# Performance work log

Hardware: AMD Instinct MI355X
Metric: run time of the kernel (lower is better)

Reference implementation:

```python
import jax, jax.numpy as jnp
from jax import lax
import numpy as np

B, T, F, H, MH = 512, 256, 8, 128, 512  # batch, horizon, exo features, lstm hidden, mlp hidden


def setup_inputs() -> dict:
    key = jax.random.key(0)
    ks = jax.random.split(key, 32)

    def u(k, shape, scale):
        return jax.random.uniform(k, shape, jnp.float32, -scale, scale)

    kH = 1.0 / np.sqrt(H)
    kM = 1.0 / np.sqrt(MH)
    inp = {}
    for i, n in enumerate(["Dis_out", "Dis_rad", "Dis_occ"]):
        inp[n] = jax.random.normal(ks[i], (B, T, F), jnp.float32)
    for j in range(3):
        b = 3 + j * 5
        inp[f"lstm{j+1}_Wih"] = u(ks[b], (4 * H, F), kH)      # torch gate order i,f,g,o
        inp[f"lstm{j+1}_Whh"] = u(ks[b + 1], (4 * H, H), kH)
        inp[f"lstm{j+1}_b"] = u(ks[b + 2], (4 * H,), kH)
        inp[f"lstm{j+1}_hw"] = u(ks[b + 3], (H,), kH)          # linear head H -> 1
        inp[f"lstm{j+1}_hb"] = u(ks[b + 4], (), kH)
    inp["mlp_W1"] = u(ks[20], (3, MH), 1.0 / np.sqrt(3.0))
    inp["mlp_b1"] = u(ks[21], (MH,), 1.0 / np.sqrt(3.0))
    inp["mlp_W2"] = u(ks[22], (MH, MH), kM)
    inp["mlp_b2"] = u(ks[23], (MH,), kM)
    inp["mlp_W3"] = u(ks[24], (MH,), kM)
    inp["mlp_b3"] = u(ks[25], (), kM)
    return inp


def _lstm_head(x, Wih, Whh, b, hw, hb):
    # x: (B,T,F) -> per-step scalar prediction (B,T)
    Bsz, Hs = x.shape[0], Whh.shape[1]

    def step(carry, xt):
        h, c = carry
        z = xt @ Wih.T + h @ Whh.T + b                 # (B,4H)
        i, f, g, o = jnp.split(z, 4, axis=-1)
        c = jax.nn.sigmoid(f) * c + jax.nn.sigmoid(i) * jnp.tanh(g)
        h = jax.nn.sigmoid(o) * jnp.tanh(c)
        return (h, c), h

    h0 = jnp.zeros((Bsz, Hs), x.dtype)
    _, hs = lax.scan(step, (h0, h0), jnp.swapaxes(x, 0, 1))  # hs: (T,B,H)
    return jnp.einsum('tbh,h->bt', hs, hw) + hb              # (B,T)


def reference(Dis_out, Dis_rad, Dis_occ,
              lstm1_Wih, lstm1_Whh, lstm1_b, lstm1_hw, lstm1_hb,
              lstm2_Wih, lstm2_Whh, lstm2_b, lstm2_hw, lstm2_hb,
              lstm3_Wih, lstm3_Whh, lstm3_b, lstm3_hw, lstm3_hb,
              mlp_W1, mlp_b1, mlp_W2, mlp_b2, mlp_W3, mlp_b3):
    D1 = _lstm_head(Dis_out, lstm1_Wih, lstm1_Whh, lstm1_b, lstm1_hw, lstm1_hb)
    D2 = _lstm_head(Dis_rad, lstm2_Wih, lstm2_Whh, lstm2_b, lstm2_hw, lstm2_hb)
    D3 = _lstm_head(Dis_occ, lstm3_Wih, lstm3_Whh, lstm3_b, lstm3_hw, lstm3_hb)
    # Batched replacement of the per-timestep loop: concat -> tiny MLP, all T at once.
    x = jnp.stack([D1, D2, D3], axis=-1)                      # (B,T,3)
    h = jax.nn.relu(x @ mlp_W1 + mlp_b1)                      # (B,T,MH)
    h = jax.nn.relu(h @ mlp_W2 + mlp_b2)                      # (B,T,MH)
    c_p_F = h @ mlp_W3 + mlp_b3                               # (B,T)
    return (D1, D2, D3, c_p_F)
```

## Files before the change

kernel.cpp:

```cpp
#include <hip/hip_runtime.h>

#define B_ 512
#define T_ 256
#define F_ 8
#define H_ 128
#define BT_ (B_*T_)
#define MH_ 512
#define L2E 1.4426950408889634f

typedef __attribute__((ext_vector_type(4))) float f32x4;
typedef __attribute__((ext_vector_type(8))) __bf16 bf16x8;

__device__ unsigned short g_w2t[MH_*MH_];
__device__ unsigned short g_whh[3][512][128];
__device__ unsigned short g_wih[3][512][32];
__device__ unsigned short g_xbf[3][B_*T_*F_];

__device__ __forceinline__ unsigned short f2bf(float f){
  unsigned int u = __float_as_uint(f);
  unsigned int r = (u + 0x7FFFu + ((u >> 16) & 1u)) >> 16;
  return (unsigned short)r;
}

#if __has_builtin(__builtin_amdgcn_exp2f)
#define EXP2F __builtin_amdgcn_exp2f
#else
#define EXP2F exp2f
#endif
#define RCPF __builtin_amdgcn_rcpf

struct LstmArgs {
  const float* x[3];
  const float* Wih[3];
  const float* Whh[3];
  const float* bias[3];
  const float* hw[3];
  const float* hb[3];
  float* out;
};

__global__ __launch_bounds__(256) void prep_lstm(LstmArgs A){
  const int NW = 3*512*128;
  const int NI = 3*512*32;
  const int NX = 3*B_*T_*F_;
  for (int i = blockIdx.x*256 + threadIdx.x; i < NW+NI+NX; i += gridDim.x*256){
    if (i < NW){
      int head = i >> 16;
      int r = i & 65535;
      int pc = r >> 7, k = r & 127;
      int w = pc >> 6, g = (pc >> 4) & 3, s = pc & 15;
      int row = g*128 + w*16 + s;
      float sc = (g == 2) ? (2.0f*L2E) : (-L2E);
      g_whh[head][pc][k] = f2bf(A.Whh[head][row*H_ + k] * sc);
    } else if (i < NW + NI){
      int j = i - NW;
      int head = j >> 14;
      int r = j & 16383;
      int pc = r >> 5, k = r & 31;
      int w = pc >> 6, g = (pc >> 4) & 3, s = pc & 15;
      int row = g*128 + w*16 + s;
      float sc = (g == 2) ? (2.0f*L2E) : (-L2E);
      g_wih[head][pc][k] = (k < 8) ? f2bf(A.Wih[head][row*F_ + k] * sc) : (unsigned short)0;
    } else {
      int j = i - NW - NI;
      int head = j >> 20;
      int r = j & 1048575;
      g_xbf[head][r] = f2bf(A.x[head][r]);
    }
  }
}

__global__ __launch_bounds__(512) void lstm_mfma_kernel(LstmArgs A){
  const int head   = blockIdx.x >> 6;
  const int batch0 = (blockIdx.x & 63) * 8;
  const int tid = threadIdx.x;
  const int w   = tid >> 6;
  const int l   = tid & 63;
  const int c16 = l & 15;
  const int kb  = (l >> 4) * 8;

  const float* __restrict__ bs  = A.bias[head];
  const float* __restrict__ hwp = A.hw[head];
  const float hbv = A.hb[head][0];
  float* __restrict__ D = A.out + (size_t)head * BT_;

  bf16x8 bh[4][4];
  bf16x8 bx[4];
  #pragma unroll
  for (int g = 0; g < 4; ++g){
    const int pc = w*64 + g*16 + c16;
    #pragma unroll
    for (int kk = 0; kk < 4; ++kk)
      bh[g][kk] = *(const bf16x8*)&g_whh[head][pc][kk*32 + kb];
    bx[g] = *(const bf16x8*)&g_wih[head][pc][kb];
  }

  const int u = w*16 + c16;
  const float bi_ = bs[u]        * (-L2E);
  const float bf_ = bs[H_+u]     * (-L2E);
  const float bg_ = bs[2*H_+u]   * (2.0f*L2E);
  const float bo_ = bs[3*H_+u]   * (-L2E);
  const float hw_u = hwp[u];

  __shared__ __align__(16) unsigned short h_bf[2][16][132];
  __shared__ float part[2][8][8];

  for (int i = tid; i < 2*16*132; i += 512) ((unsigned short*)h_bf)[i] = 0;

  float cst[2] = {0.f, 0.f};
  float pp[2]  = {0.f, 0.f};

  const int bt = ((c16 >> 2) << 1) | (c16 & 1);
  const bool xvalid = (l < 16) && !(l & 2);
  const unsigned short* __restrict__ xrow =
      &g_xbf[head][(size_t)(batch0 + bt) * (T_*F_)];

  bf16x8 ax_cur = {};
  if (xvalid) ax_cur = *(const bf16x8*)(xrow);

  __syncthreads();

  int cur = 0;
  for (int ts = 0; ts < T_; ++ts){
    bf16x8 ah[4];
    #pragma unroll
    for (int kk = 0; kk < 4; ++kk)
      ah[kk] = *(const bf16x8*)&h_bf[cur][c16][kk*32 + kb];

    bf16x8 ax_nxt = {};
    {
      const int tn = (ts + 1 < T_) ? ts + 1 : ts;
      if (xvalid) ax_nxt = *(const bf16x8*)(xrow + tn*F_);
    }

    f32x4 acc[4];
    const f32x4 z4 = {0.f, 0.f, 0.f, 0.f};
    #pragma unroll
    for (int g = 0; g < 4; ++g)
      acc[g] = __builtin_amdgcn_mfma_f32_16x16x32_bf16(ah[0], bh[g][0], z4, 0, 0, 0);
    #pragma unroll
    for (int kk = 1; kk < 4; ++kk){
      #pragma unroll
      for (int g = 0; g < 4; ++g)
        acc[g] = __builtin_amdgcn_mfma_f32_16x16x32_bf16(ah[kk], bh[g][kk], acc[g], 0, 0, 0);
    }
    #pragma unroll
    for (int g = 0; g < 4; ++g)
      acc[g] = __builtin_amdgcn_mfma_f32_16x16x32_bf16(ax_cur, bx[g], acc[g], 0, 0, 0);

    if (ts > 0){
      #pragma unroll
      for (int r = 0; r < 2; ++r){
        float v = pp[r];
        v += __shfl_xor(v, 1); v += __shfl_xor(v, 2);
        v += __shfl_xor(v, 4); v += __shfl_xor(v, 8);
        if (c16 == 0) part[(ts-1) & 1][(l >> 4)*2 + r][w] = v;
      }
    }

    #pragma unroll
    for (int r = 0; r < 2; ++r){
      const float Zi = acc[0][r] + bi_;
      const float Zf = acc[1][r] + bf_;
      const float Zg = acc[2][r] + bg_;
      const float Zo = acc[3][r] + bo_;
      const float si = RCPF(1.f + EXP2F(Zi));
      const float sf = RCPF(1.f + EXP2F(Zf));
      const float tg = 1.f - 2.f * RCPF(EXP2F(Zg) + 1.f);
      const float so = RCPF(1.f + EXP2F(Zo));
      cst[r] = sf * cst[r] + si * tg;
      const float tc = 1.f - 2.f * RCPF(EXP2F(cst[r] * (2.0f*L2E)) + 1.f);
      const float hnr = so * tc;
      h_bf[cur ^ 1][(l >> 4)*4 + r][u] = f2bf(hnr);
      pp[r] = hnr * hw_u;
    }

    __syncthreads();

    if (ts > 0 && tid < 64){
      const int b  = tid >> 3;
      const int wv = tid & 7;
      float v = part[(ts-1) & 1][b][wv];
      v += __shfl_xor(v, 1); v += __shfl_xor(v, 2); v += __shfl_xor(v, 4);
      if (wv == 0) D[(size_t)(batch0 + b) * T_ + (ts-1)] = v + hbv;
    }

    ax_cur = ax_nxt;
    cur ^= 1;
  }

  #pragma unroll
  for (int r = 0; r < 2; ++r){
    float v = pp[r];
    v += __shfl_xor(v, 1); v += __shfl_xor(v, 2);
    v += __shfl_xor(v, 4); v += __shfl_xor(v, 8);
    if (c16 == 0) part[(T_-1) & 1][(l >> 4)*2 + r][w] = v;
  }
  __syncthreads();
  if (tid < 64){
    const int b  = tid >> 3;
    const int wv = tid & 7;
    float v = part[(T_-1) & 1][b][wv];
    v += __shfl_xor(v, 1); v += __shfl_xor(v, 2); v += __shfl_xor(v, 4);
    if (wv == 0) D[(size_t)(batch0 + b) * T_ + (T_-1)] = v + hbv;
  }
}

__global__ __launch_bounds__(256) void prep_w2t(const float* __restrict__ W2){
  const int idx = blockIdx.x * 256 + threadIdx.x;
  const int n = idx >> 9;
  const int k = idx & 511;
  g_w2t[(n << 9) | (k ^ ((n & 7) << 3))] = f2bf(W2[(size_t)k * MH_ + n]);
}

__global__ __launch_bounds__(256, 2) void mlp_kernel(
    const float* __restrict__ Dbase,
    const float* __restrict__ W1, const float* __restrict__ b1,
    const float* __restrict__ b2, const float* __restrict__ W3,
    const float* __restrict__ b3, float* __restrict__ out)
{
  __shared__ __align__(16) unsigned short buf[2][32*512];

  const int tid = threadIdx.x;
  const int l   = tid & 63;
  const int c16 = l & 15;
  const int kb  = (l >> 4) * 8;
  const int w   = tid >> 6;
  const int m0  = blockIdx.x * 128 + w * 32;

  bf16x8 afr[2][16];
  {
    float d[2][3];
    #pragma unroll
    for (int mt = 0; mt < 2; ++mt){
      const int gr = m0 + mt*16 + c16;
      d[mt][0] = Dbase[gr];
      d[mt][1] = Dbase[BT_ + gr];
      d[mt][2] = Dbase[2*BT_ + gr];
    }
    #pragma unroll
    for (int ks = 0; ks < 16; ++ks){
      const int kg = ks*32 + kb;
      const f32x4 wa0 = *(const f32x4*)(W1 + kg);          const f32x4 wa1 = *(const f32x4*)(W1 + kg + 4);
      const f32x4 wb0 = *(const f32x4*)(W1 + MH_ + kg);    const f32x4 wb1 = *(const f32x4*)(W1 + MH_ + kg + 4);
      const f32x4 wc0 = *(const f32x4*)(W1 + 2*MH_ + kg);  const f32x4 wc1 = *(const f32x4*)(W1 + 2*MH_ + kg + 4);
      const f32x4 bv0 = *(const f32x4*)(b1 + kg);          const f32x4 bv1 = *(const f32x4*)(b1 + kg + 4);
      #pragma unroll
      for (int mt = 0; mt < 2; ++mt){
        union { unsigned short us[8]; bf16x8 v; } au;
        #pragma unroll
        for (int i = 0; i < 4; ++i){
          float v0 = fmaf(d[mt][2], wc0[i], fmaf(d[mt][1], wb0[i], fmaf(d[mt][0], wa0[i], bv0[i])));
          float v1 = fmaf(d[mt][2], wc1[i], fmaf(d[mt][1], wb1[i], fmaf(d[mt][0], wa1[i], bv1[i])));
          au.us[i]     = f2bf(fmaxf(v0, 0.f));
          au.us[4 + i] = f2bf(fmaxf(v1, 0.f));
        }
        afr[mt][ks] = au.v;
      }
    }
  }

  const uint4* __restrict__ gsrc = (const uint4*)g_w2t;
  uint4 rg0, rg1, rg2, rg3, rg4, rg5, rg6, rg7;
  {
    const uint4* s = gsrc + tid;
    rg0 = s[0*256]; rg1 = s[1*256]; rg2 = s[2*256]; rg3 = s[3*256];
    rg4 = s[4*256]; rg5 = s[5*256]; rg6 = s[6*256]; rg7 = s[7*256];
  }

  float rs[2][4] = {{0.f,0.f,0.f,0.f},{0.f,0.f,0.f,0.f}};

  #pragma unroll 1
  for (int p = 0; p < 16; ++p){
    {
      uint4* bw = (uint4*)buf[p & 1] + tid;
      bw[0*256] = rg0; bw[1*256] = rg1; bw[2*256] = rg2; bw[3*256] = rg3;
      bw[4*256] = rg4; bw[5*256] = rg5; bw[6*256] = rg6; bw[7*256] = rg7;
    }
    __syncthreads();
    if (p < 15){
      const uint4* s = gsrc + (p + 1) * 2048 + tid;
      rg0 = s[0*256]; rg1 = s[1*256]; rg2 = s[2*256]; rg3 = s[3*256];
      rg4 = s[4*256]; rg5 = s[5*256]; rg6 = s[6*256]; rg7 = s[7*256];
    }
    float b2v[2], w3v[2];
    #pragma unroll
    for (int nt = 0; nt < 2; ++nt){
      const int n = p*32 + nt*16 + c16;
      b2v[nt] = b2[n];
      w3v[nt] = W3[n];
    }

    const unsigned short* __restrict__ bb = buf[p & 1];
    f32x4 acc[2][2];
    #pragma unroll
    for (int nt = 0; nt < 2; ++nt){
      f32x4 z = {0.f,0.f,0.f,0.f};
      acc[0][nt] = z; acc[1][nt] = z;
    }
    #pragma unroll
    for (int ks = 0; ks < 16; ++ks){
      #pragma unroll
      for (int nt = 0; nt < 2; ++nt){
        const int nl = nt*16 + c16;
        const bf16x8 bfr =
          *(const bf16x8*)&bb[(nl << 9) | ((ks*32 + kb) ^ ((nl & 7) << 3))];
        acc[0][nt] = __builtin_amdgcn_mfma_f32_16x16x32_bf16(afr[0][ks], bfr, acc[0][nt], 0, 0, 0);
        acc[1][nt] = __builtin_amdgcn_mfma_f32_16x16x32_bf16(afr[1][ks], bfr, acc[1][nt], 0, 0, 0);
      }
    }
    #pragma unroll
    for (int nt = 0; nt < 2; ++nt){
      #pragma unroll
      for (int mt = 0; mt < 2; ++mt)
        #pragma unroll
        for (int r = 0; r < 4; ++r)
          rs[mt][r] += fmaxf(acc[mt][nt][r] + b2v[nt], 0.f) * w3v[nt];
    }
  }

  #pragma unroll
  for (int mt = 0; mt < 2; ++mt){
    #pragma unroll
    for (int r = 0; r < 4; ++r){
      rs[mt][r] += __shfl_xor(rs[mt][r], 1);
      rs[mt][r] += __shfl_xor(rs[mt][r], 2);
      rs[mt][r] += __shfl_xor(rs[mt][r], 4);
      rs[mt][r] += __shfl_xor(rs[mt][r], 8);
    }
  }
  if (c16 == 0){
    const float bv = b3[0];
    #pragma unroll
    for (int mt = 0; mt < 2; ++mt){
      const int row = m0 + mt*16 + (l >> 4) * 4;
      #pragma unroll
      for (int r = 0; r < 4; ++r)
        out[3*BT_ + row + r] = rs[mt][r] + bv;
    }
  }
}

extern "C" void kernel_launch(void* const* d_in, const int* in_sizes, int n_in,
                              void* d_out, int out_size, void* d_ws, size_t ws_size,
                              hipStream_t stream){
  LstmArgs A;
  for (int i = 0; i < 3; ++i){
    A.x[i]    = (const float*)d_in[i];
    A.Wih[i]  = (const float*)d_in[3 + i*5 + 0];
    A.Whh[i]  = (const float*)d_in[3 + i*5 + 1];
    A.bias[i] = (const float*)d_in[3 + i*5 + 2];
    A.hw[i]   = (const float*)d_in[3 + i*5 + 3];
    A.hb[i]   = (const float*)d_in[3 + i*5 + 4];
  }
  A.out = (float*)d_out;

  prep_w2t<<<dim3(1024), dim3(256), 0, stream>>>((const float*)d_in[20]);
  prep_lstm<<<dim3(2048), dim3(256), 0, stream>>>(A);
  lstm_mfma_kernel<<<dim3(192), dim3(512), 0, stream>>>(A);
  mlp_kernel<<<dim3(1024), dim3(256), 0, stream>>>((const float*)d_out,
      (const float*)d_in[18], (const float*)d_in[19],
      (const float*)d_in[21], (const float*)d_in[22], (const float*)d_in[23],
      (float*)d_out);
}
```

Baseline: 329.5 us.

## Compute LSTM head projection via MFMA in wave 0 and fold bias into accumulators

Replaces the per-step shuffle reduction plus shared-memory partial-sum stage for the linear head with an extra MFMA chain in wave 0. That chain multiplies the bf16 hidden state just read from LDS by a padded bf16 head-weight matrix, and the head bias is used as the initial accumulator. Gate biases are likewise preloaded into the MFMA accumulators, and the bf16 conversion uses the hardware cast. This removes the shuffles, the partial-sum buffer and the post-barrier reduction from the serial recurrence. The cost is some imbalance, since wave 0 does extra MFMA work, and the head now sees h in bf16 instead of fp32.

```diff
diff --git a/kernel.cpp b/kernel.cpp
--- a/kernel.cpp
+++ b/kernel.cpp
@@ -15,11 +15,17 @@
 __device__ unsigned short g_whh[3][512][128];
 __device__ unsigned short g_wih[3][512][32];
 __device__ unsigned short g_xbf[3][B_*T_*F_];
+__device__ unsigned short g_hwd[3][16][128];
 
 __device__ __forceinline__ unsigned short f2bf(float f){
   unsigned int u = __float_as_uint(f);
   unsigned int r = (u + 0x7FFFu + ((u >> 16) & 1u)) >> 16;
   return (unsigned short)r;
+}
+__device__ __forceinline__ unsigned short cvt_bf16(float f){
+  union { __bf16 b; unsigned short u; } c;
+  c.b = (__bf16)f;
+  return c.u;
 }
 
 #if __has_builtin(__builtin_amdgcn_exp2f)
@@ -43,7 +49,8 @@
   const int NW = 3*512*128;
   const int NI = 3*512*32;
   const int NX = 3*B_*T_*F_;
-  for (int i = blockIdx.x*256 + threadIdx.x; i < NW+NI+NX; i += gridDim.x*256){
+  const int NH = 3*16*128;
+  for (int i = blockIdx.x*256 + threadIdx.x; i < NW+NI+NX+NH; i += gridDim.x*256){
     if (i < NW){
       int head = i >> 16;
       int r = i & 65535;
@@ -61,11 +68,17 @@
       int row = g*128 + w*16 + s;
       float sc = (g == 2) ? (2.0f*L2E) : (-L2E);
       g_wih[head][pc][k] = (k < 8) ? f2bf(A.Wih[head][row*F_ + k] * sc) : (unsigned short)0;
-    } else {
+    } else if (i < NW + NI + NX){
       int j = i - NW - NI;
       int head = j >> 20;
       int r = j & 1048575;
       g_xbf[head][r] = f2bf(A.x[head][r]);
+    } else {
+      int j = i - NW - NI - NX;
+      int head = j >> 11;
+      int r = j & 2047;
+      int col = r >> 7, k = r & 127;
+      g_hwd[head][col][k] = (col == 0) ? f2bf(A.hw[head][k]) : (unsigned short)0;
     }
   }
 }
@@ -80,7 +93,6 @@
   const int kb  = (l >> 4) * 8;
 
   const float* __restrict__ bs  = A.bias[head];
-  const float* __restrict__ hwp = A.hw[head];
   const float hbv = A.hb[head][0];
   float* __restrict__ D = A.out + (size_t)head * BT_;
 
@@ -94,38 +106,47 @@
       bh[g][kk] = *(const bf16x8*)&g_whh[head][pc][kk*32 + kb];
     bx[g] = *(const bf16x8*)&g_wih[head][pc][kb];
   }
+  bf16x8 bD[4];
+  if (w == 0){
+    #pragma unroll
+    for (int kk = 0; kk < 4; ++kk)
+      bD[kk] = *(const bf16x8*)&g_hwd[head][c16][kk*32 + kb];
+  }
 
   const int u = w*16 + c16;
   const float bi_ = bs[u]        * (-L2E);
   const float bf_ = bs[H_+u]     * (-L2E);
   const float bg_ = bs[2*H_+u]   * (2.0f*L2E);
   const float bo_ = bs[3*H_+u]   * (-L2E);
-  const float hw_u = hwp[u];
 
   __shared__ __align__(16) unsigned short h_bf[2][16][132];
-  __shared__ float part[2][8][8];
 
   for (int i = tid; i < 2*16*132; i += 512) ((unsigned short*)h_bf)[i] = 0;
 
   float cst[2] = {0.f, 0.f};
-  float pp[2]  = {0.f, 0.f};
+
+  unsigned short* const hb0 = &h_bf[0][0][0];
+  const int rdbase = c16*132 + kb;
+  const int wrbase = ((l >> 4)*4)*132 + u;
+  int curo = 0;
 
   const int bt = ((c16 >> 2) << 1) | (c16 & 1);
   const bool xvalid = (l < 16) && !(l & 2);
   const unsigned short* __restrict__ xrow =
       &g_xbf[head][(size_t)(batch0 + bt) * (T_*F_)];
 
+  float* __restrict__ Dp = D + (size_t)(batch0 + 2*(l >> 4)) * T_;
+
   bf16x8 ax_cur = {};
   if (xvalid) ax_cur = *(const bf16x8*)(xrow);
 
   __syncthreads();
 
-  int cur = 0;
   for (int ts = 0; ts < T_; ++ts){
     bf16x8 ah[4];
     #pragma unroll
     for (int kk = 0; kk < 4; ++kk)
-      ah[kk] = *(const bf16x8*)&h_bf[cur][c16][kk*32 + kb];
+      ah[kk] = *(const bf16x8*)(hb0 + curo + rdbase + kk*32);
 
     bf16x8 ax_nxt = {};
     {
@@ -134,12 +155,12 @@
     }
 
     f32x4 acc[4];
-    const f32x4 z4 = {0.f, 0.f, 0.f, 0.f};
-    #pragma unroll
-    for (int g = 0; g < 4; ++g)
-      acc[g] = __builtin_amdgcn_mfma_f32_16x16x32_bf16(ah[0], bh[g][0], z4, 0, 0, 0);
-    #pragma unroll
-    for (int kk = 1; kk < 4; ++kk){
+    acc[0] = (f32x4){bi_, bi_, bi_, bi_};
+    acc[1] = (f32x4){bf_, bf_, bf_, bf_};
+    acc[2] = (f32x4){bg_, bg_, bg_, bg_};
+    acc[3] = (f32x4){bo_, bo_, bo_, bo_};
+    #pragma unroll
+    for (int kk = 0; kk < 4; ++kk){
       #pragma unroll
       for (int g = 0; g < 4; ++g)
         acc[g] = __builtin_amdgcn_mfma_f32_16x16x32_bf16(ah[kk], bh[g][kk], acc[g], 0, 0, 0);
@@ -148,61 +169,47 @@
     for (int g = 0; g < 4; ++g)
       acc[g] = __builtin_amdgcn_mfma_f32_16x16x32_bf16(ax_cur, bx[g], acc[g], 0, 0, 0);
 
-    if (ts > 0){
-      #pragma unroll
-      for (int r = 0; r < 2; ++r){
-        float v = pp[r];
-        v += __shfl_xor(v, 1); v += __shfl_xor(v, 2);
-        v += __shfl_xor(v, 4); v += __shfl_xor(v, 8);
-        if (c16 == 0) part[(ts-1) & 1][(l >> 4)*2 + r][w] = v;
+    if (w == 0){
+      f32x4 accD = {hbv, hbv, hbv, hbv};
+      #pragma unroll
+      for (int kk = 0; kk < 4; ++kk)
+        accD = __builtin_amdgcn_mfma_f32_16x16x32_bf16(ah[kk], bD[kk], accD, 0, 0, 0);
+      if (ts > 0 && c16 == 0){
+        Dp[ts-1]      = accD[0];
+        Dp[T_ + ts-1] = accD[1];
       }
     }
 
+    unsigned short* const hw_ptr = hb0 + (curo ^ 2112) + wrbase;
     #pragma unroll
     for (int r = 0; r < 2; ++r){
-      const float Zi = acc[0][r] + bi_;
-      const float Zf = acc[1][r] + bf_;
-      const float Zg = acc[2][r] + bg_;
-      const float Zo = acc[3][r] + bo_;
-      const float si = RCPF(1.f + EXP2F(Zi));
-      const float sf = RCPF(1.f + EXP2F(Zf));
-      const float tg = 1.f - 2.f * RCPF(EXP2F(Zg) + 1.f);
-      const float so = RCPF(1.f + EXP2F(Zo));
+      const float si = RCPF(1.f + EXP2F(acc[0][r]));
+      const float sf = RCPF(1.f + EXP2F(acc[1][r]));
+      const float tg = 1.f - 2.f * RCPF(EXP2F(acc[2][r]) + 1.f);
+      const float so = RCPF(1.f + EXP2F(acc[3][r]));
       cst[r] = sf * cst[r] + si * tg;
       const float tc = 1.f - 2.f * RCPF(EXP2F(cst[r] * (2.0f*L2E)) + 1.f);
-      const float hnr = so * tc;
-      h_bf[cur ^ 1][(l >> 4)*4 + r][u] = f2bf(hnr);
-      pp[r] = hnr * hw_u;
+      hw_ptr[r*132] = cvt_bf16(so * tc);
     }
 
     __syncthreads();
-
-    if (ts > 0 && tid < 64){
-      const int b  = tid >> 3;
-      const int wv = tid & 7;
-      float v = part[(ts-1) & 1][b][wv];
-      v += __shfl_xor(v, 1); v += __shfl_xor(v, 2); v += __shfl_xor(v, 4);
-      if (wv == 0) D[(size_t)(batch0 + b) * T_ + (ts-1)] = v + hbv;
-    }
-
+    curo ^= 2112;
     ax_cur = ax_nxt;
-    cur ^= 1;
-  }
-
-  #pragma unroll
-  for (int r = 0; r < 2; ++r){
-    float v = pp[r];
-    v += __shfl_xor(v, 1); v += __shfl_xor(v, 2);
-    v += __shfl_xor(v, 4); v += __shfl_xor(v, 8);
-    if (c16 == 0) part[(T_-1) & 1][(l >> 4)*2 + r][w] = v;
-  }
-  __syncthreads();
-  if (tid < 64){
-    const int b  = tid >> 3;
-    const int wv = tid & 7;
-    float v = part[(T_-1) & 1][b][wv];
-    v += __shfl_xor(v, 1); v += __shfl_xor(v, 2); v += __shfl_xor(v, 4);
-    if (wv == 0) D[(size_t)(batch0 + b) * T_ + (T_-1)] = v + hbv;
+  }
+
+  if (w == 0){
+    bf16x8 ah[4];
+    #pragma unroll
+    for (int kk = 0; kk < 4; ++kk)
+      ah[kk] = *(const bf16x8*)(hb0 + curo + rdbase + kk*32);
+    f32x4 accD = {hbv, hbv, hbv, hbv};
+    #pragma unroll
+    for (int kk = 0; kk < 4; ++kk)
+      accD = __builtin_amdgcn_mfma_f32_16x16x32_bf16(ah[kk], bD[kk], accD, 0, 0, 0);
+    if (c16 == 0){
+      Dp[T_-1]      = accD[0];
+      Dp[T_ + T_-1] = accD[1];
+    }
   }
 }
 
```

New measurement: 385.1 us. 16.9% more time.
